# Kernel optimization log

Hardware: AMD Instinct MI355X
Metric: run time of the kernel (lower is better)

Reference implementation:

```python
import jax, jax.numpy as jnp
import numpy as np

N_NODES = 50000
N_EDGES = 1600000
D = 128


def setup_inputs() -> dict:
    key = jax.random.key(0)
    k1, k2, k3, k4 = jax.random.split(key, 4)
    x = jax.random.normal(k1, (N_NODES, D), dtype=jnp.float32)
    src = jax.random.randint(k2, (N_EDGES,), 0, N_NODES, dtype=jnp.int64)
    dst = jax.random.randint(k3, (N_EDGES,), 0, N_NODES, dtype=jnp.int64)
    # Linear(2*D, 1): weight [2*D, 1] (transposed vs torch), bias [1]
    W = jax.random.normal(k4, (2 * D, 1), dtype=jnp.float32) * (1.0 / np.sqrt(2 * D))
    b = jnp.zeros((1,), dtype=jnp.float32)
    return {"x": x, "src": src, "dst": dst, "W": W, "b": b}


def reference(x, src, dst, W, b):
    # score_e = W^T [x[src_e]; x[dst_e]] + b
    # Equivalent split form avoids materializing the [E, 2D] concat when possible,
    # but stays mathematically identical to cat + Linear.
    Ws, Wd = W[:D], W[D:]            # [D,1] each
    xs = x @ Ws                       # [N,1] per-node src contribution
    xd = x @ Wd                       # [N,1] per-node dst contribution
    score = xs[src] + xd[dst] + b     # [E,1]
    return score
```

## Files before the change

kernel.cpp:

```cpp
#include <hip/hip_runtime.h>
#include <hip/hip_bf16.h>

#define DDIM 128
#define K2_BLOCKS 256
#define K2_THREADS 1024
#define MAX_TAB32 25088

typedef float vf4 __attribute__((ext_vector_type(4)));
typedef int   vi4 __attribute__((ext_vector_type(4)));

__device__ __forceinline__ float bf16_to_f32(unsigned short u) {
    return __uint_as_float(((unsigned int)u) << 16);
}

__device__ __forceinline__ void lds_dma16(const void* g, void* l) {
    __builtin_amdgcn_global_load_lds(
        (const __attribute__((address_space(1))) unsigned int*)g,
        (__attribute__((address_space(3))) unsigned int*)l,
        16, 0, 0);
}

__global__ __launch_bounds__(256) void node_proj_kernel(
    const float* __restrict__ x,
    const float* __restrict__ W,
    __hip_bfloat16* __restrict__ xs,
    __hip_bfloat16* __restrict__ xd,
    int n_nodes)
{
    const int tib  = threadIdx.x;
    const int lane = tib & 63;
    const int w    = blockIdx.x * 4 + (tib >> 6);
    const int c    = lane & 15;
    const int r    = lane >> 4;

    const vf4 wsA = *reinterpret_cast<const vf4*>(W + c * 8);
    const vf4 wsB = *reinterpret_cast<const vf4*>(W + c * 8 + 4);
    const vf4 wdA = *reinterpret_cast<const vf4*>(W + DDIM + c * 8);
    const vf4 wdB = *reinterpret_cast<const vf4*>(W + DDIM + c * 8 + 4);

    const int ra = 8 * w + r;
    const int rb = ra + 4;
    vf4 a0 = {0,0,0,0}, a1 = {0,0,0,0};
    vf4 b0 = {0,0,0,0}, b1 = {0,0,0,0};
    if (ra < n_nodes) {
        const vf4* pa = reinterpret_cast<const vf4*>(x + (size_t)ra * DDIM + c * 8);
        a0 = __builtin_nontemporal_load(pa);
        a1 = __builtin_nontemporal_load(pa + 1);
    }
    if (rb < n_nodes) {
        const vf4* pb = reinterpret_cast<const vf4*>(x + (size_t)rb * DDIM + c * 8);
        b0 = __builtin_nontemporal_load(pb);
        b1 = __builtin_nontemporal_load(pb + 1);
    }

    float sA = a0.x*wsA.x + a0.y*wsA.y + a0.z*wsA.z + a0.w*wsA.w
             + a1.x*wsB.x + a1.y*wsB.y + a1.z*wsB.z + a1.w*wsB.w;
    float dA = a0.x*wdA.x + a0.y*wdA.y + a0.z*wdA.z + a0.w*wdA.w
             + a1.x*wdB.x + a1.y*wdB.y + a1.z*wdB.z + a1.w*wdB.w;
    float sB = b0.x*wsA.x + b0.y*wsA.y + b0.z*wsA.z + b0.w*wsA.w
             + b1.x*wsB.x + b1.y*wsB.y + b1.z*wsB.z + b1.w*wsB.w;
    float dB = b0.x*wdA.x + b0.y*wdA.y + b0.z*wdA.z + b0.w*wdA.w
             + b1.x*wdB.x + b1.y*wdB.y + b1.z*wdB.z + b1.w*wdB.w;

    #pragma unroll
    for (int m = 8; m >= 1; m >>= 1) {
        sA += __shfl_xor(sA, m, 64);
        dA += __shfl_xor(dA, m, 64);
        sB += __shfl_xor(sB, m, 64);
        dB += __shfl_xor(dB, m, 64);
    }
    if (c == 0) {
        if (ra < n_nodes) {
            xs[ra] = __float2bfloat16(sA);
            xd[ra] = __float2bfloat16(dA);
        }
        if (rb < n_nodes) {
            xs[rb] = __float2bfloat16(sB);
            xd[rb] = __float2bfloat16(dB);
        }
    }
}

__global__ __launch_bounds__(K2_THREADS) void edge_lds_kernel(
    const int* __restrict__ src,
    const int* __restrict__ dst,
    const unsigned char* __restrict__ xs_b,
    const unsigned char* __restrict__ xd_b,
    const float* __restrict__ b,
    float* __restrict__ out,
    int nb, int n_quads, int n_edges)
{
    __shared__ __align__(16) unsigned short tab[MAX_TAB32 * 2];
    unsigned char* tabb = reinterpret_cast<unsigned char*>(tab);

    const int tid = threadIdx.x;
    const int wv  = tid >> 6;
    const int ln  = tid & 63;
    const int gid = blockIdx.x * K2_THREADS + tid;
    const int T   = K2_BLOCKS * K2_THREADS;

    const int q0 = gid, q1 = gid + T;
    const bool h0 = q0 < n_quads, h1 = q1 < n_quads;
    vi4 s0 = {0,0,0,0}, s1 = {0,0,0,0};
    vi4 t0 = {0,0,0,0}, t1 = {0,0,0,0};
    if (h0) {
        s0 = __builtin_nontemporal_load(reinterpret_cast<const vi4*>(src) + q0);
        t0 = __builtin_nontemporal_load(reinterpret_cast<const vi4*>(dst) + q0);
    }
    if (h1) {
        s1 = __builtin_nontemporal_load(reinterpret_cast<const vi4*>(src) + q1);
        t1 = __builtin_nontemporal_load(reinterpret_cast<const vi4*>(dst) + q1);
    }
    const float bb = b[0];

    for (int i = wv; i < nb; i += K2_THREADS / 64)
        lds_dma16(xs_b + (size_t)i * 1024 + ln * 16, tabb + i * 1024);
    __syncthreads();

    vf4 p0 = {0,0,0,0}, p1 = {0,0,0,0};
    if (h0) {
        p0.x = bf16_to_f32(tab[s0.x]) + bb;
        p0.y = bf16_to_f32(tab[s0.y]) + bb;
        p0.z = bf16_to_f32(tab[s0.z]) + bb;
        p0.w = bf16_to_f32(tab[s0.w]) + bb;
    }
    if (h1) {
        p1.x = bf16_to_f32(tab[s1.x]) + bb;
        p1.y = bf16_to_f32(tab[s1.y]) + bb;
        p1.z = bf16_to_f32(tab[s1.z]) + bb;
        p1.w = bf16_to_f32(tab[s1.w]) + bb;
    }
    const int tail = n_edges & 3;
    int te = -1; float pt = 0.f; int td = 0;
    if (blockIdx.x == 0 && tid < tail) {
        te = (n_quads << 2) + tid;
        td = dst[te];
        pt = bf16_to_f32(tab[reinterpret_cast<const unsigned short*>(xs_b)[0] == 0
                             ? src[te] : src[te]]) + bb;
    }

    __syncthreads();
    for (int i = wv; i < nb; i += K2_THREADS / 64)
        lds_dma16(xd_b + (size_t)i * 1024 + ln * 16, tabb + i * 1024);
    __syncthreads();

    if (h0) {
        vf4 o;
        o.x = p0.x + bf16_to_f32(tab[t0.x]);
        o.y = p0.y + bf16_to_f32(tab[t0.y]);
        o.z = p0.z + bf16_to_f32(tab[t0.z]);
        o.w = p0.w + bf16_to_f32(tab[t0.w]);
        __builtin_nontemporal_store(o, reinterpret_cast<vf4*>(out) + q0);
    }
    if (h1) {
        vf4 o;
        o.x = p1.x + bf16_to_f32(tab[t1.x]);
        o.y = p1.y + bf16_to_f32(tab[t1.y]);
        o.z = p1.z + bf16_to_f32(tab[t1.z]);
        o.w = p1.w + bf16_to_f32(tab[t1.w]);
        __builtin_nontemporal_store(o, reinterpret_cast<vf4*>(out) + q1);
    }
    if (te >= 0) out[te] = pt + bf16_to_f32(tab[td]);
}

extern "C" void kernel_launch(void* const* d_in, const int* in_sizes, int n_in,
                              void* d_out, int out_size, void* d_ws, size_t ws_size,
                              hipStream_t stream) {
    const float* x   = (const float*)d_in[0];
    const int*   src = (const int*)d_in[1];
    const int*   dst = (const int*)d_in[2];
    const float* W   = (const float*)d_in[3];
    const float* b   = (const float*)d_in[4];
    float* out = (float*)d_out;

    const int n_nodes = in_sizes[0] / DDIM;
    const int n_edges = in_sizes[1];

    const int n32 = (n_nodes + 1) >> 1;
    const int nb  = (n32 * 4 + 1023) >> 10;
    unsigned char* wsb = (unsigned char*)d_ws;
    __hip_bfloat16* xs = (__hip_bfloat16*)wsb;
    __hip_bfloat16* xd = (__hip_bfloat16*)(wsb + (size_t)nb * 1024);

    const int k1_blocks = (n_nodes + 31) >> 5;
    node_proj_kernel<<<k1_blocks, 256, 0, stream>>>(x, W, xs, xd, n_nodes);

    const int n_quads = n_edges >> 2;
    edge_lds_kernel<<<K2_BLOCKS, K2_THREADS, 0, stream>>>(
        src, dst, wsb, wsb + (size_t)nb * 1024, b, out,
        nb, n_quads, n_edges);
}
```

Measured before the change: 16.85 us.

## Preload xs table and first part of xd table together into LDS

The edge kernel previously loaded the full xs table into LDS, gathered, synced, then reloaded the whole xd table. Now it loads xs plus the first 61KB of xd into a larger LDS buffer up front, gathers both, then only loads the remaining part of xd after the second barrier. This shortens the serialized second load phase, at the cost of more LDS per block (159KB), branches on each dst index, and a second gather pass split by index range.

```diff
diff --git a/kernel.cpp b/kernel.cpp
--- a/kernel.cpp
+++ b/kernel.cpp
@@ -4,7 +4,8 @@
 #define DDIM 128
 #define K2_BLOCKS 256
 #define K2_THREADS 1024
-#define MAX_TAB32 25088
+#define MAX_XS_UNITS 98
+#define TABB_UNITS   61
 
 typedef float vf4 __attribute__((ext_vector_type(4)));
 typedef int   vi4 __attribute__((ext_vector_type(4)));
@@ -88,10 +89,13 @@
     const unsigned char* __restrict__ xd_b,
     const float* __restrict__ b,
     float* __restrict__ out,
-    int nb, int n_quads, int n_edges)
+    int units, int loU, int hiU, int split, int n_quads, int n_edges)
 {
-    __shared__ __align__(16) unsigned short tab[MAX_TAB32 * 2];
-    unsigned char* tabb = reinterpret_cast<unsigned char*>(tab);
+    __shared__ __align__(16) unsigned char lds[(MAX_XS_UNITS + TABB_UNITS) * 1024];
+    unsigned char* tabA = lds;
+    unsigned char* tabB = lds + MAX_XS_UNITS * 1024;
+    const unsigned short* tA16 = reinterpret_cast<const unsigned short*>(tabA);
+    const unsigned short* tB16 = reinterpret_cast<const unsigned short*>(tabB);
 
     const int tid = threadIdx.x;
     const int wv  = tid >> 6;
@@ -112,55 +116,69 @@
         t1 = __builtin_nontemporal_load(reinterpret_cast<const vi4*>(dst) + q1);
     }
     const float bb = b[0];
-
-    for (int i = wv; i < nb; i += K2_THREADS / 64)
-        lds_dma16(xs_b + (size_t)i * 1024 + ln * 16, tabb + i * 1024);
+    const int tail = n_edges & 3;
+    int te = -1, ts = 0, td = 0; float pt = 0.f;
+    if (blockIdx.x == 0 && tid < tail) {
+        te = (n_quads << 2) + tid;
+        ts = src[te];
+        td = dst[te];
+    }
+
+    for (int i = wv; i < units; i += K2_THREADS / 64)
+        lds_dma16(xs_b + (size_t)i * 1024 + ln * 16, tabA + i * 1024);
+    for (int i = wv; i < loU; i += K2_THREADS / 64)
+        lds_dma16(xd_b + (size_t)i * 1024 + ln * 16, tabB + i * 1024);
     __syncthreads();
 
     vf4 p0 = {0,0,0,0}, p1 = {0,0,0,0};
     if (h0) {
-        p0.x = bf16_to_f32(tab[s0.x]) + bb;
-        p0.y = bf16_to_f32(tab[s0.y]) + bb;
-        p0.z = bf16_to_f32(tab[s0.z]) + bb;
-        p0.w = bf16_to_f32(tab[s0.w]) + bb;
+        p0.x = bf16_to_f32(tA16[s0.x]) + bb;
+        p0.y = bf16_to_f32(tA16[s0.y]) + bb;
+        p0.z = bf16_to_f32(tA16[s0.z]) + bb;
+        p0.w = bf16_to_f32(tA16[s0.w]) + bb;
+        if (t0.x < split) p0.x += bf16_to_f32(tB16[t0.x]);
+        if (t0.y < split) p0.y += bf16_to_f32(tB16[t0.y]);
+        if (t0.z < split) p0.z += bf16_to_f32(tB16[t0.z]);
+        if (t0.w < split) p0.w += bf16_to_f32(tB16[t0.w]);
     }
     if (h1) {
-        p1.x = bf16_to_f32(tab[s1.x]) + bb;
-        p1.y = bf16_to_f32(tab[s1.y]) + bb;
-        p1.z = bf16_to_f32(tab[s1.z]) + bb;
-        p1.w = bf16_to_f32(tab[s1.w]) + bb;
-    }
-    const int tail = n_edges & 3;
-    int te = -1; float pt = 0.f; int td = 0;
-    if (blockIdx.x == 0 && tid < tail) {
-        te = (n_quads << 2) + tid;
-        td = dst[te];
-        pt = bf16_to_f32(tab[reinterpret_cast<const unsigned short*>(xs_b)[0] == 0
-                             ? src[te] : src[te]]) + bb;
+        p1.x = bf16_to_f32(tA16[s1.x]) + bb;
+        p1.y = bf16_to_f32(tA16[s1.y]) + bb;
+        p1.z = bf16_to_f32(tA16[s1.z]) + bb;
+        p1.w = bf16_to_f32(tA16[s1.w]) + bb;
+        if (t1.x < split) p1.x += bf16_to_f32(tB16[t1.x]);
+        if (t1.y < split) p1.y += bf16_to_f32(tB16[t1.y]);
+        if (t1.z < split) p1.z += bf16_to_f32(tB16[t1.z]);
+        if (t1.w < split) p1.w += bf16_to_f32(tB16[t1.w]);
+    }
+    if (te >= 0) {
+        pt = bf16_to_f32(tA16[ts]) + bb;
+        if (td < split) pt += bf16_to_f32(tB16[td]);
     }
 
     __syncthreads();
-    for (int i = wv; i < nb; i += K2_THREADS / 64)
-        lds_dma16(xd_b + (size_t)i * 1024 + ln * 16, tabb + i * 1024);
+    for (int i = wv; i < hiU; i += K2_THREADS / 64)
+        lds_dma16(xd_b + (size_t)(loU + i) * 1024 + ln * 16, tabA + i * 1024);
     __syncthreads();
 
     if (h0) {
-        vf4 o;
-        o.x = p0.x + bf16_to_f32(tab[t0.x]);
-        o.y = p0.y + bf16_to_f32(tab[t0.y]);
-        o.z = p0.z + bf16_to_f32(tab[t0.z]);
-        o.w = p0.w + bf16_to_f32(tab[t0.w]);
-        __builtin_nontemporal_store(o, reinterpret_cast<vf4*>(out) + q0);
+        if (t0.x >= split) p0.x += bf16_to_f32(tA16[t0.x - split]);
+        if (t0.y >= split) p0.y += bf16_to_f32(tA16[t0.y - split]);
+        if (t0.z >= split) p0.z += bf16_to_f32(tA16[t0.z - split]);
+        if (t0.w >= split) p0.w += bf16_to_f32(tA16[t0.w - split]);
+        __builtin_nontemporal_store(p0, reinterpret_cast<vf4*>(out) + q0);
     }
     if (h1) {
-        vf4 o;
-        o.x = p1.x + bf16_to_f32(tab[t1.x]);
-        o.y = p1.y + bf16_to_f32(tab[t1.y]);
-        o.z = p1.z + bf16_to_f32(tab[t1.z]);
-        o.w = p1.w + bf16_to_f32(tab[t1.w]);
-        __builtin_nontemporal_store(o, reinterpret_cast<vf4*>(out) + q1);
-    }
-    if (te >= 0) out[te] = pt + bf16_to_f32(tab[td]);
+        if (t1.x >= split) p1.x += bf16_to_f32(tA16[t1.x - split]);
+        if (t1.y >= split) p1.y += bf16_to_f32(tA16[t1.y - split]);
+        if (t1.z >= split) p1.z += bf16_to_f32(tA16[t1.z - split]);
+        if (t1.w >= split) p1.w += bf16_to_f32(tA16[t1.w - split]);
+        __builtin_nontemporal_store(p1, reinterpret_cast<vf4*>(out) + q1);
+    }
+    if (te >= 0) {
+        if (td >= split) pt += bf16_to_f32(tA16[td - split]);
+        out[te] = pt;
+    }
 }
 
 extern "C" void kernel_launch(void* const* d_in, const int* in_sizes, int n_in,
@@ -176,17 +194,19 @@
     const int n_nodes = in_sizes[0] / DDIM;
     const int n_edges = in_sizes[1];
 
-    const int n32 = (n_nodes + 1) >> 1;
-    const int nb  = (n32 * 4 + 1023) >> 10;
+    const int units = (n_nodes * 2 + 1023) >> 10;
+    const int loU   = units < TABB_UNITS ? units : TABB_UNITS;
+    const int hiU   = units - loU;
+    const int split = loU * 512;
     unsigned char* wsb = (unsigned char*)d_ws;
     __hip_bfloat16* xs = (__hip_bfloat16*)wsb;
-    __hip_bfloat16* xd = (__hip_bfloat16*)(wsb + (size_t)nb * 1024);
+    __hip_bfloat16* xd = (__hip_bfloat16*)(wsb + (size_t)units * 1024);
 
     const int k1_blocks = (n_nodes + 31) >> 5;
     node_proj_kernel<<<k1_blocks, 256, 0, stream>>>(x, W, xs, xd, n_nodes);
 
     const int n_quads = n_edges >> 2;
     edge_lds_kernel<<<K2_BLOCKS, K2_THREADS, 0, stream>>>(
-        src, dst, wsb, wsb + (size_t)nb * 1024, b, out,
-        nb, n_quads, n_edges);
-}
+        src, dst, wsb, wsb + (size_t)units * 1024, b, out,
+        units, loU, hiU, split, n_quads, n_edges);
+}
```

Result: slower. 17.81 us (+5.7%).
